# Performance work log

Hardware: AMD Instinct MI355X
Metric: run time of the kernel (lower is better)

Reference implementation:

```python
import jax, jax.numpy as jnp
import numpy as np

NQ, NT, NRF, K, M, B = 8, 16, 4, 4, 2, 28
N_OUTER, N_INNER = 120, 20

def _ry(t):
    c, s = jnp.cos(t / 2), jnp.sin(t / 2)
    return jnp.stack([jnp.stack([c, -s]), jnp.stack([s, c])]).astype(jnp.complex64)

def _rz(t):
    e = jnp.exp(-0.5j * t)
    z = jnp.zeros_like(e)
    return jnp.stack([jnp.stack([e, z]), jnp.stack([z, jnp.conj(e)])])

def _rot(phi, theta, omega):  # pennylane Rot = RZ(omega) RY(theta) RZ(phi)
    return _rz(omega) @ _ry(theta) @ _rz(phi)

def _ap1(state, U, w):
    return jnp.moveaxis(jnp.tensordot(U, state, axes=[[1], [w]]), 0, w)

def _cnot(state, c, t):
    s = jnp.moveaxis(state, (c, t), (0, 1))
    s = s.at[1].set(s[1, ::-1])
    return jnp.moveaxis(s, (0, 1), (c, t))

def _qcircuit(inp, w):  # inp [2*NQ] angles, w [3,NQ,3] -> [NQ] PauliZ expvals
    st = jnp.zeros((2,) * NQ, jnp.complex64).at[(0,) * NQ].set(1.0)
    for i in range(NQ):
        st = _ap1(st, _ry(inp[i]), i)
        st = _ap1(st, _rz(inp[i + NQ]), i)
    for l in range(3):
        for i in range(NQ):
            st = _ap1(st, _rot(w[l, i, 0], w[l, i, 1], w[l, i, 2]), i)
        for i in range(NQ - 1):
            st = _cnot(st, i, i + 1)
        st = _cnot(st, NQ - 1, 0)
    p = jnp.abs(st) ** 2
    z = [jnp.moveaxis(p, i, 0)[0].sum() - jnp.moveaxis(p, i, 0)[1].sum() for i in range(NQ)]
    return jnp.stack(z).astype(jnp.float32)

def _qblock(x, p):  # x [B,80] -> [B,out]
    W1, b1, W2, b2, W3, b3, qw, Wp, bp = p
    h = jnp.tanh(x @ W1.T + b1)
    h = jnp.tanh(h @ W2.T + b2)
    ang = h @ W3.T + b3  # [B, 2*NQ]
    q = jax.vmap(_qcircuit, in_axes=(0, None))(ang, qw)  # [B, NQ]
    return q @ Wp.T + bp

def _to_complex(x):
    return x[..., 0::2] + 1j * x[..., 1::2]

def _sum_rate(H, F, W, Pt):
    Heff = jnp.einsum('kbmn,nbr,kbru->kbmu', H, F[0], W)  # [K,B,M,M]
    G = jnp.einsum('kbmu,kbvu->kbmv', Heff, jnp.conj(Heff))
    A = jnp.eye(M, dtype=G.dtype) + Pt * G
    return jnp.sum(jnp.log2(jnp.abs(jnp.linalg.det(A).real) + 1e-12), axis=0).astype(jnp.float32)

def _beam_err(H, F, W, R, Pt):
    X = jnp.einsum('nbr,kbru->kbnu', F[0], W)  # [K,B,NT,M]
    C = jnp.einsum('kbnu,kbvu->kbnv', X, jnp.conj(X))  # [K,B,NT,NT]
    return jnp.mean(jnp.sqrt(jnp.sum(jnp.abs(C - R) ** 2, axis=(2, 3)) + 1e-12), axis=0).astype(jnp.float32)

def _normalize(F, W, H, Pt):
    F = F / (jnp.abs(F) + 1e-12)
    X = jnp.einsum('nbr,kbru->kbnu', F[0], W)
    pw = jnp.sum(jnp.abs(X) ** 2, axis=(0, 2, 3))  # [B]
    return F, W * jnp.sqrt(Pt / (pw + 1e-12))[None, :, None, None]

def _initialize(H, R, Pt, key):
    k1, k2 = jax.random.split(key)
    ph = jax.random.uniform(k1, (1, NT, B, NRF), maxval=2 * np.pi)
    F = jnp.exp(1j * ph).astype(jnp.complex64)
    W = jax.random.normal(k2, (K, B, NRF, M), dtype=jnp.complex64)
    return _normalize(F, W, H, Pt)

def _state(H, F, W, R, Wproj, bproj):
    s = jnp.concatenate([
        jnp.abs(F).mean((0, 1)).reshape(-1),    # B*NRF
        jnp.angle(F).mean((0, 1)).reshape(-1),  # B*NRF
        jnp.abs(W).mean((0, 1, 2)),             # M
        jnp.angle(W).mean((0, 1, 2)),           # M
        jnp.abs(H).mean((0, 1, 2)).reshape(-1), # NT
        jnp.abs(R).mean((0, 1)).reshape(-1),    # NT*NT  -> total 500
    ])
    return jnp.broadcast_to(s @ Wproj.T + bproj, (B, Wproj.shape[0]))

def _forward(H, R, Pt, step, qFp, qWp, Wproj, bproj):
    F, W = _initialize(H, R, Pt, jax.random.key(1))
    r0, t0 = _sum_rate(H, F, W, Pt), _beam_err(H, F, W, R, Pt)
    base = jax.random.key(7)

    def outer(carry, it):
        F, W = carry
        k = jax.random.fold_in(base, it)
        st = _state(H, F, W, R, Wproj, bproj)  # [B,80]

        def inner(c, p):
            Fc, kk = c
            kk, kn = jax.random.split(kk)
            dF = _to_complex(_qblock(st, p)).reshape(B, NT, NRF).transpose(1, 0, 2)[None]
            noise = jax.random.normal(kn, Fc.shape, dtype=jnp.complex64)
            Fc = Fc + step * noise * 0.001 + dF * 0.001
            return (Fc / (jnp.abs(Fc) + 1e-12), kk), None

        (F, k), _ = jax.lax.scan(inner, (F, k), qFp)
        dW = _to_complex(_qblock(st, qWp)).reshape(B, K, NRF, M).transpose(1, 0, 2, 3)
        k, kn = jax.random.split(k)
        W = W + step * jax.random.normal(kn, W.shape, dtype=jnp.complex64) * 0.001 + dW * 0.001
        F, W = _normalize(F, W, H, Pt)
        return (F, W), (_sum_rate(H, F, W, Pt), _beam_err(H, F, W, R, Pt))

    (F, W), (rs, ts) = jax.lax.scan(outer, (F, W), jnp.arange(N_OUTER))
    rates = jnp.concatenate([r0[None], rs], axis=0).T  # [B, N_OUTER+1]
    taus = jnp.concatenate([t0[None], ts], axis=0).T
    return rates, taus, F, W


def setup_inputs() -> dict:
    key = jax.random.key(0)
    ks = jax.random.split(key, 32)
    r = lambda i, sh: jax.random.normal(ks[i], sh, dtype=jnp.float32)
    WS = 0.1  # weight init scale for tanh stability
    return {
        'H_re': r(0, (K, B, M, NT)), 'H_im': r(1, (K, B, M, NT)),
        'R_re': r(2, (K, B, NT, NT)), 'R_im': r(3, (K, B, NT, NT)),
        'Pt': jnp.ones((1,), jnp.float32),
        'step': jnp.ones((1,), jnp.float32) * 0.02,
        'qF_W1': r(4, (N_INNER, 64, 80)) * WS, 'qF_b1': r(5, (N_INNER, 64)) * WS,
        'qF_W2': r(6, (N_INNER, 32, 64)) * WS, 'qF_b2': r(7, (N_INNER, 32)) * WS,
        'qF_W3': r(8, (N_INNER, 16, 32)) * WS, 'qF_b3': r(9, (N_INNER, 16)) * WS,
        'qF_qw': r(10, (N_INNER, 3, NQ, 3)), 'qF_Wp': r(11, (N_INNER, 128, NQ)) * WS,
        'qF_bp': r(12, (N_INNER, 128)) * WS,
        'qW_W1': r(13, (64, 80)) * WS, 'qW_b1': r(14, (64,)) * WS,
        'qW_W2': r(15, (32, 64)) * WS, 'qW_b2': r(16, (32,)) * WS,
        'qW_W3': r(17, (16, 32)) * WS, 'qW_b3': r(18, (16,)) * WS,
        'qW_qw': r(19, (3, NQ, 3)), 'qW_Wp': r(20, (64, NQ)) * WS,
        'qW_bp': r(21, (64,)) * WS,
        'proj_W': r(22, (80, 500)) * WS, 'proj_b': r(23, (80,)) * WS,
    }


def reference(H_re, H_im, R_re, R_im, Pt, step, qF_W1, qF_b1, qF_W2, qF_b2, qF_W3, qF_b3,
              qF_qw, qF_Wp, qF_bp, qW_W1, qW_b1, qW_W2, qW_b2, qW_W3, qW_b3, qW_qw, qW_Wp,
              qW_bp, proj_W, proj_b):
    H = (H_re + 1j * H_im).astype(jnp.complex64)
    R = (R_re + 1j * R_im).astype(jnp.complex64)
    qFp = (qF_W1, qF_b1, qF_W2, qF_b2, qF_W3, qF_b3, qF_qw, qF_Wp, qF_bp)
    qWp = (qW_W1, qW_b1, qW_W2, qW_b2, qW_W3, qW_b3, qW_qw, qW_Wp, qW_bp)
    return _forward(H, R, Pt[0], step[0], qFp, qWp, proj_W, proj_b)
```

## Files before the change

### kernel.cpp

```cpp
#include <hip/hip_runtime.h>
#include <stdint.h>

#define NT_   16
#define NRF_  4
#define K_    4
#define M_    2
#define B_    28
#define NOUT_ 120
#define NIN_  20
#define FN_   1792
#define WN_   896
#define XN_   3584
#define TJOB_ 8704
#define TSZ_  (21*TJOB_)
#define O_TAUS 3388
#define O_F    6776
#define O_W    10360

typedef float2 cf;
__device__ __forceinline__ cf cmul(cf a, cf b){ return make_float2(a.x*b.x - a.y*b.y, a.x*b.y + a.y*b.x); }
__device__ __forceinline__ cf cmulc(cf a, cf b){ return make_float2(a.x*b.x + a.y*b.y, a.y*b.x - a.x*b.y); }
__device__ __forceinline__ cf cadd(cf a, cf b){ return make_float2(a.x + b.x, a.y + b.y); }
__device__ __forceinline__ cf csc(float s, cf a){ return make_float2(s*a.x, s*a.y); }
__device__ __forceinline__ cf shflc(cf v, int m){ return make_float2(__shfl_xor(v.x, m, 64), __shfl_xor(v.y, m, 64)); }
// ... 130 lines not shown
    const float TWOPI = 6.28318530717958647692f;
    for (int e = t; e < FN_; e += 1024){
      float u = bits_to_unit(rbits(keys[0], (uint32_t)e));
      float ph = fmaxf(0.0f, u * TWOPI);
      float s, c; sincosf(ph, &s, &c);
      wsFst[e] = make_float2(c, s);
    }
    for (int e = t; e < WN_; e += 1024){
      cf w = cnormal(keys[1], keys[2], (uint32_t)e);
      wsIW[e] = w;
      wsWst[e] = w;
    }
  } else if (bi < 4*NOUT_ + 1 + 21){
    const int j = bi - (4*NOUT_ + 1);
    const bool isW = (j == 20);
    const float* W1 = isW ? qW_W1 : qF_W1 + j*(64*80);
    const float* W2 = isW ? qW_W2 : qF_W2 + j*(32*64);
    const float* W3 = isW ? qW_W3 : qF_W3 + j*(16*32);
    const float* Wp = isW ? qW_Wp : qF_Wp + j*(128*8);
    float* dst = wsT + j*TJOB_;
    for (int idx = t; idx < 5120; idx += 1024){
      int q = idx >> 6, i = idx & 63;
      dst[idx] = W1[i*80 + q];
    }
    for (int idx = t; idx < 2048; idx += 1024){
      int q = idx >> 5, i = idx & 31;
      dst[5120 + idx] = W2[i*64 + q];
    }
    for (int idx = t; idx < 512; idx += 1024){
      int q = idx >> 4, i = idx & 15;
      dst[7168 + idx] = W3[i*32 + q];
    }
    const int nOut = isW ? 64 : 128;
    for (int idx = t; idx < 8*nOut; idx += 1024){
      int z = idx / nOut, o = idx - z*nOut;
      dst[7680 + z*128 + o] = Wp[o*8 + z];
    }
  } else {
    if (t < 504){
      int j = t / 24, gg = t - j*24;
      const float* qw = (j == 20) ? qW_qw : qF_qw + j*72;
      float phi = qw[gg*3], th = qw[gg*3 + 1], om = qw[gg*3 + 2];
      float sh, ch; sincosf(0.5f*th, &sh, &ch);
      float sp, cp; sincosf(0.5f*(phi + om), &sp, &cp);
      float sm, cm; sincosf(0.5f*(phi - om), &sm, &cm);
      float* u = wsU + t*8;
      u[0] =  ch*cp; u[1] = -ch*sp;
      u[2] = -sh*cm; u[3] = -sh*sm;
      u[4] =  sh*cm; u[5] = -sh*sm;
      u[6] =  ch*cp; u[7] =  ch*sp;
    } else if (t < 520){
      int n = t - 504;
      float s = 0.f;
      for (int kbm = 0; kbm < 224; ++kbm){
        float re = H_re[kbm*16 + n], im = H_im[kbm*16 + n];
        s += sqrtf(re*re + im*im);
      }
      wsC[n] = s * (1.0f/224.0f);
    } else if (t < 776){
      int nv = t - 520;
      float s = 0.f;
      for (int kb = 0; kb < 112; ++kb){
        float re = R_re[kb*256 + nv], im = R_im[kb*256 + nv];
        s += sqrtf(re*re + im*im);
      }
      wsC[16 + nv] = s * (1.0f/112.0f);
    }
  }
}

__device__ __forceinline__ void gate(int q, cf u00, cf u01, cf u10, cf u11,
                                     cf &a0, cf &a1, cf &a2, cf &a3, int lane){
  if (q == 7){
    cf n0 = cadd(cmul(u00, a0), cmul(u01, a1));
    cf n1 = cadd(cmul(u10, a0), cmul(u11, a1));
    cf n2 = cadd(cmul(u00, a2), cmul(u01, a3));
    cf n3 = cadd(cmul(u10, a2), cmul(u11, a3));
    a0 = n0; a1 = n1; a2 = n2; a3 = n3;
  } else if (q == 6){
    cf n0 = cadd(cmul(u00, a0), cmul(u01, a2));
    cf n2 = cadd(cmul(u10, a0), cmul(u11, a2));
    cf n1 = cadd(cmul(u00, a1), cmul(u01, a3));
    cf n3 = cadd(cmul(u10, a1), cmul(u11, a3));
    a0 = n0; a1 = n1; a2 = n2; a3 = n3;
  } else {
    const int m = 1 << (5 - q);
    const bool hi = (lane & m) != 0;
    cf cO = hi ? u11 : u00;
    cf cP = hi ? u10 : u01;
    cf p0 = shflc(a0, m), p1 = shflc(a1, m), p2 = shflc(a2, m), p3 = shflc(a3, m);
    a0 = cadd(cmul(cO, a0), cmul(cP, p0));
    a1 = cadd(cmul(cO, a1), cmul(cP, p1));
    a2 = cadd(cmul(cO, a2), cmul(cP, p2));
    a3 = cadd(cmul(cO, a3), cmul(cP, p3));
  }
}

__device__ void run_circuit2(const float* trig, const float* uni, int lane, float z[8]){
  cf a0 = make_float2(lane == 0 ? 1.f : 0.f, 0.f);
  cf a1 = make_float2(0.f, 0.f), a2 = make_float2(0.f, 0.f), a3 = make_float2(0.f, 0.f);
  #pragma unroll
  for (int i = 0; i < 8; ++i){
    float sh = trig[2*i],      ch = trig[2*i + 1];
    float sp = trig[16 + 2*i], cp = trig[16 + 2*i + 1];
    float sm = trig[32 + 2*i], cm = trig[32 + 2*i + 1];
    cf u00 = make_float2( ch*cp, -ch*sp);
    cf u11 = make_float2( ch*cp,  ch*sp);
    cf u01 = make_float2(-sh*cm, -sh*sm);
    cf u10 = make_float2( sh*cm, -sh*sm);
    gate(i, u00, u01, u10, u11, a0, a1, a2, a3, lane);
  }
  for (int l = 0; l < 3; ++l){
    #pragma unroll
    for (int i = 0; i < 8; ++i){
      const float* u = uni + (l*8 + i)*8;
      gate(i, make_float2(u[0], u[1]), make_float2(u[2], u[3]),
              make_float2(u[4], u[5]), make_float2(u[6], u[7]), a0, a1, a2, a3, lane);
    }
    #pragma unroll
    for (int i = 0; i < 5; ++i){
      const int cm_ = 1 << (5 - i), tm = 1 << (4 - i);
      const bool c = (lane & cm_) != 0;
      cf p0 = shflc(a0, tm), p1 = shflc(a1, tm), p2 = shflc(a2, tm), p3 = shflc(a3, tm);
      a0 = c ? p0 : a0; a1 = c ? p1 : a1; a2 = c ? p2 : a2; a3 = c ? p3 : a3;
    }
    {
      const bool c = (lane & 1) != 0;
      cf t0 = c ? a2 : a0, t2 = c ? a0 : a2;
      cf t1 = c ? a3 : a1, t3 = c ? a1 : a3;
      a0 = t0; a1 = t1; a2 = t2; a3 = t3;
    }
    { cf tmp = a2; a2 = a3; a3 = tmp; }
    a1 = shflc(a1, 32);
    a3 = shflc(a3, 32);
  }
  const float p0 = a0.x*a0.x + a0.y*a0.y;
  const float p1 = a1.x*a1.x + a1.y*a1.y;
  const float p2 = a2.x*a2.x + a2.y*a2.y;
  const float p3 = a3.x*a3.x + a3.y*a3.y;
  const float tot = p0 + p1 + p2 + p3;
  z[6] = (p0 + p1) - (p2 + p3);
  z[7] = (p0 + p2) - (p1 + p3);
  #pragma unroll
  for (int i = 0; i < 6; ++i)
    z[i] = ((lane >> (5 - i)) & 1) ? -tot : tot;
  #pragma unroll
  for (int m = 1; m < 64; m <<= 1){
    #pragma unroll
    for (int i = 0; i < 8; ++i) z[i] += __shfl_xor(z[i], m, 64);
  }
}

__global__ __launch_bounds__(640)
void k_iter(const float* __restrict__ H_re, const float* __restrict__ H_im,
            const float* __restrict__ R_re, const float* __restrict__ R_im,
            const float* __restrict__ Pt_p, const float* __restrict__ step_p,
            const float* __restrict__ wsT, const float* __restrict__ wsU,
            const float* __restrict__ wsC,
            const float* __restrict__ featInA, const float* __restrict__ featInG,
            const float* __restrict__ featInP,
            float* __restrict__ featOutA, float* __restrict__ featOutG,
            float* __restrict__ featOutP,
            const float* __restrict__ projW, const float* __restrict__ projB,
            const float* __restrict__ qF_b1, const float* __restrict__ qF_b2,
            const float* __restrict__ qF_b3, const float* __restrict__ qF_bp,
            const float* __restrict__ qW_b1, const float* __restrict__ qW_b2,
            const float* __restrict__ qW_b3, const float* __restrict__ qW_bp,
            const float2* __restrict__ wsF, const float2* __restrict__ wsW,
            float2* __restrict__ wsdF, float2* __restrict__ wsdW,
            float2* __restrict__ wsFst, float2* __restrict__ wsWst,
            uint32_t* __restrict__ flag, uint32_t target,
            float* __restrict__ out, int it)
{
  const int wg = blockIdx.x;
  const int t = threadIdx.x;
  const int lane = t & 63;
  const int wv = t >> 6;
  __shared__ float sS[500];
  __shared__ float sSt[80];
  __shared__ float mlp[160];
  __shared__ float luni[192];
  __shared__ cf lF[64];
  __shared__ cf lW[32];
  __shared__ cf lX[128];
  __shared__ float scrA[96], scrG[96];
  __shared__ float red2[2];
  __shared__ float sscale;
  __shared__ float heR[16], heI[16];
  __shared__ float sKBl[4], sKB2l[4];

  if (wg < 21){
    const int j = wg;
    const bool isW = (j == 20);
    for (int i = t; i < 192; i += 640) luni[i] = wsU[j*192 + i];
    for (int i = t; i < 112; i += 640){ sS[i] = featInA[i]; sS[112 + i] = featInG[i]; }
    if (t < 4){
      float s = 0.f;
      for (int bb = 0; bb < 28; ++bb) s += featInP[bb*4 + t];
      sS[224 + t] = s * (1.0f/448.0f);
    }
    for (int i = t; i < 272; i += 640) sS[228 + i] = wsC[i];
    __syncthreads();
    {
      int o = wv*8 + (lane >> 3), i = lane & 7;
      const float* row = projW + o*500;
      float acc = 0.f;
      #pragma unroll
      for (int s = 0; s < 63; ++s){
        int j2 = i + 8*s;
        if (j2 < 500) acc = fmaf(sS[j2], row[j2], acc);
      }
      #pragma unroll
      for (int m = 1; m < 8; m <<= 1) acc += __shfl_xor(acc, m, 64);
      if (i == 0) sSt[o] = acc + projB[o];
    }
    __syncthreads();
    if (t < 64){
      const float* b1 = isW ? qW_b1 : qF_b1 + j*64;
      const float* b2 = isW ? qW_b2 : qF_b2 + j*32;
      const float* b3 = isW ? qW_b3 : qF_b3 + j*16;
      const float* bp = isW ? qW_bp : qF_bp + j*128;
      const float* w1t = wsT + j*TJOB_;
      const float* w2t = w1t + 5120;
      const float* w3t = w1t + 7168;
      const float* wpt = w1t + 7680;
      {
        float acc = b1[lane];
        for (int q = 0; q < 80; ++q) acc = fmaf(w1t[q*64 + lane], sSt[q], acc);
        mlp[lane] = tanhf(acc);
      }
      __builtin_amdgcn_wave_barrier();
      {
        int i2 = lane & 31;
        float acc = b2[i2];
        for (int q = 0; q < 64; ++q) acc = fmaf(w2t[q*32 + i2], mlp[q], acc);
        float h2 = tanhf(acc);
        __builtin_amdgcn_wave_barrier();
        if (lane < 32) mlp[64 + lane] = h2;
      }
      __builtin_amdgcn_wave_barrier();
      {
        int i3 = lane & 15;
        float acc = b3[i3];
        for (int q = 0; q < 32; ++q) acc = fmaf(w3t[q*16 + i3], mlp[64 + q], acc);
        __builtin_amdgcn_wave_barrier();
        if (lane < 16) mlp[96 + lane] = acc;
      }
      __builtin_amdgcn_wave_barrier();
      if (lane < 24){
        int i = lane & 7, which = lane >> 3;
        float th = mlp[96 + i], om = mlp[96 + 8 + i];
        float arg = (which == 0) ? 0.5f*th
                  : (which == 1) ? 0.5f*(0.f + om)
                                 : 0.5f*(0.f - om);
        float s, c; sincosf(arg, &s, &c);
        mlp[112 + which*16 + 2*i]     = s;
        mlp[112 + which*16 + 2*i + 1] = c;
      }
      __builtin_amdgcn_wave_barrier();
      float z[8];
      run_circuit2(mlp + 112, luni, lane, z);
      if (!isW){
        float o0 = bp[lane];
        float o1 = bp[64 + lane];
        #pragma unroll
        for (int i = 0; i < 8; ++i){
          o0 = fmaf(wpt[i*128 + lane],      z[i], o0);
          o1 = fmaf(wpt[i*128 + 64 + lane], z[i], o1);
        }
        __builtin_amdgcn_wave_barrier();
        mlp[lane] = o0; mlp[64 + lane] = o1;
        __builtin_amdgcn_wave_barrier();
        wsdF[j*64 + lane] = make_float2(mlp[2*lane], mlp[2*lane + 1]);
      } else {
        float o0 = bp[lane];
        #pragma unroll
        for (int i = 0; i < 8; ++i) o0 = fmaf(wpt[i*128 + lane], z[i], o0);
        __builtin_amdgcn_wave_barrier();
        mlp[lane] = o0;
        __builtin_amdgcn_wave_barrier();
        if (lane < 32) wsdW[lane] = make_float2(mlp[2*lane], mlp[2*lane + 1]);
      }
    }
    __syncthreads();
    if (t == 0){
      __threadfence();
      __hip_atomic_fetch_add(flag, 1u, __ATOMIC_RELAXED, __HIP_MEMORY_SCOPE_AGENT);
    }
    return;
  }

  const int b = wg - 21;
  const float c1 = step_p[0] * 0.001f;
  const float Ptv = Pt_p[0];

  cf F;
  cf nzA[10], nzB[10];
  cf w, nw;
  if (t < 64){
    const int n = t >> 2, r = t & 3;
    const int e = n*112 + b*4 + r;
    F = wsFst[e];
    const float2* np = wsF + (size_t)it*(NIN_*FN_);
    #pragma unroll
    for (int s = 0; s < 10; ++s) nzA[s] = np[s*FN_ + e];
    #pragma unroll
    for (int s = 0; s < 10; ++s) nzB[s] = np[(10 + s)*FN_ + e];
  } else if (t < 96){
    const int wi = t - 64;
    const int k = wi >> 3, ru = wi & 7;
    const int ew = (k*28 + b)*8 + ru;
    w  = wsWst[ew];
    nw = wsW[(size_t)it*WN_ + ew];
  }
  if (t == 0){
    while (__hip_atomic_load(flag, __ATOMIC_RELAXED, __HIP_MEMORY_SCOPE_AGENT) < target)
      __builtin_amdgcn_s_sleep(1);
    __threadfence();
  }
  __syncthreads();

  if (t < 64){
    cf dvA[10], dvB[10];
    #pragma unroll
    for (int s = 0; s < 10; ++s) dvA[s] = wsdF[s*64 + t];
    #pragma unroll
    for (int s = 0; s < 10; ++s) dvB[s] = wsdF[(10 + s)*64 + t];
    #pragma unroll
    for (int s = 0; s < 10; ++s){
      F.x = F.x + c1*nzA[s].x + 0.001f*dvA[s].x;
      F.y = F.y + c1*nzA[s].y + 0.001f*dvA[s].y;
      float rr = sqrtf(F.x*F.x + F.y*F.y) + 1e-12f;
      F.x /= rr; F.y /= rr;
    }
    #pragma unroll
    for (int s = 0; s < 10; ++s){
      F.x = F.x + c1*nzB[s].x + 0.001f*dvB[s].x;
      F.y = F.y + c1*nzB[s].y + 0.001f*dvB[s].y;
      float rr = sqrtf(F.x*F.x + F.y*F.y) + 1e-12f;
      F.x /= rr; F.y /= rr;
    }
    float rr = sqrtf(F.x*F.x + F.y*F.y) + 1e-12f;
    F.x /= rr; F.y /= rr;
    lF[t] = F;
    const int e = (t >> 2)*112 + b*4 + (t & 3);
    wsFst[e] = F;
  } else if (t < 96){
    const int wi = t - 64;
    const int k = wi >> 3, ru = wi & 7;
    cf dw = wsdW[k*8 + ru];
    w.x = w.x + c1*nw.x + 0.001f*dw.x;
    w.y = w.y + c1*nw.y + 0.001f*dw.y;
    lW[wi] = w;
  }
  __syncthreads();
  if (t < 128){
    int u = t & 1, n = (t >> 1) & 15, k = t >> 5;
    const cf* fr = lF + n*4;
    const cf* wr = lW + k*8 + u;
    cf acc = cmul(fr[0], wr[0]);
    acc = cadd(acc, cmul(fr[1], wr[2]));
    acc = cadd(acc, cmul(fr[2], wr[4]));
    acc = cadd(acc, cmul(fr[3], wr[6]));
    lX[t] = acc;
  }
  __syncthreads();
  if (t < 128){
    float s = lX[t].x*lX[t].x + lX[t].y*lX[t].y;
    #pragma unroll
    for (int m = 1; m < 64; m <<= 1) s += __shfl_xor(s, m, 64);
    if ((t & 63) == 0) red2[t >> 6] = s;
  }
  __syncthreads();
  if (t == 0) sscale = sqrtf(Ptv / ((red2[0] + red2[1]) + 1e-12f));
  __syncthreads();
  const float sc = sscale;
  if (t < 32){
    const int k = t >> 3, ru = t & 7;
    const int ew = (k*28 + b)*8 + ru;
    cf ww = csc(sc, lW[t]);
    lW[t] = ww;
    wsWst[ew] = ww;
  }
  if (t < 128) lX[t] = csc(sc, lX[t]);
  __syncthreads();
  if (t < 16){
    const int k = t >> 2, ent = t & 3;
    const int m = ent >> 1, u = ent & 1;
    const float* hr = H_re + (k*28 + b)*32 + m*16;
    const float* hi = H_im + (k*28 + b)*32 + m*16;
    cf He = make_float2(0.f, 0.f);
    for (int n = 0; n < 16; ++n){
      cf h = make_float2(hr[n], hi[n]);
      He = cadd(He, cmul(h, lX[k*32 + n*2 + u]));
    }
    heR[t] = He.x; heI[t] = He.y;
  }
  __builtin_amdgcn_wave_barrier();
  if (t < 4){
    const int k = t;
    cf He00 = make_float2(heR[k*4 + 0], heI[k*4 + 0]);
    cf He01 = make_float2(heR[k*4 + 1], heI[k*4 + 1]);
    cf He10 = make_float2(heR[k*4 + 2], heI[k*4 + 2]);
    cf He11 = make_float2(heR[k*4 + 3], heI[k*4 + 3]);
    cf G00 = cadd(cmulc(He00, He00), cmulc(He01, He01));
    cf G01 = cadd(cmulc(He00, He10), cmulc(He01, He11));
    cf G10 = cadd(cmulc(He10, He00), cmulc(He11, He01));
    cf G11 = cadd(cmulc(He10, He10), cmulc(He11, He11));
    cf A00 = make_float2(1.f + Ptv*G00.x, Ptv*G00.y);
    cf A01 = csc(Ptv, G01);
    cf A10 = csc(Ptv, G10);
    cf A11 = make_float2(1.f + Ptv*G11.x, Ptv*G11.y);
    float detre = (A00.x*A11.x - A00.y*A11.y) - (A01.x*A10.x - A01.y*A10.y);
    sKBl[k] = log2f(fabsf(detre) + 1e-12f);
  }
  if (t < 128){
    const int k = t >> 5, i = t & 31;
    const float* rr = R_re + (k*28 + b)*256;
    const float* ri = R_im + (k*28 + b)*256;
    float acc = 0.f;
    #pragma unroll
    for (int c = 0; c < 8; ++c){
      int nv = c*32 + i;
      int n = nv >> 4, v = nv & 15;
      cf xn0 = lX[k*32 + n*2], xn1 = lX[k*32 + n*2 + 1];
      cf xv0 = lX[k*32 + v*2], xv1 = lX[k*32 + v*2 + 1];
      cf C = cadd(cmulc(xn0, xv0), cmulc(xn1, xv1));
      float dr = C.x - rr[nv], di = C.y - ri[nv];
      acc += dr*dr + di*di;
    }
    #pragma unroll
    for (int m = 1; m < 32; m <<= 1) acc += __shfl_xor(acc, m, 64);
    if (i == 0) sKB2l[k] = sqrtf(acc + 1e-12f);
  }
  __syncthreads();
  if (t == 0){
    const int slot = it + 1;
    out[b*121 + slot] = sKBl[0] + sKBl[1] + sKBl[2] + sKBl[3];
    out[O_TAUS + b*121 + slot] = 0.25f*(sKB2l[0] + sKB2l[1] + sKB2l[2] + sKB2l[3]);
  }
  if (t < 64){
    cf f = lF[t];
    scrA[t] = sqrtf(f.x*f.x + f.y*f.y);
    scrG[t] = atan2f(f.y, f.x);
  } else if (t < 96){
    cf ww = lW[t - 64];
    scrA[t] = sqrtf(ww.x*ww.x + ww.y*ww.y);
    scrG[t] = atan2f(ww.y, ww.x);
  }
  __syncthreads();
  if (t < 8){
    int r = t & 3;
    const float* src = (t < 4) ? scrA : scrG;
    float s = 0.f;
    for (int n = 0; n < 16; ++n) s += src[n*4 + r];
    float* dst = (t < 4) ? featOutA : featOutG;
    dst[b*4 + r] = s * (1.0f/16.0f);
  } else if (t >= 8 && t < 12){
    int tt = t - 8;
    int u = tt & 1; bool isG = tt >= 2;
    const float* src = isG ? scrG : scrA;
    float s = 0.f;
    for (int i = 0; i < 16; ++i) s += src[64 + i*2 + u];
    featOutP[b*4 + tt] = s;
  }
}

__global__ __launch_bounds__(128)
void k_update(const float* __restrict__ H_re, const float* __restrict__ H_im,
              const float* __restrict__ R_re, const float* __restrict__ R_im,
              const float* __restrict__ Pt_p, const float* __restrict__ step_p,
              float2* __restrict__ wsFst, float2* __restrict__ wsWst,
              float* __restrict__ wsFeatA, float* __restrict__ wsFeatG,
              float* __restrict__ wsPart,
              float* __restrict__ out){
  const int b = blockIdx.x;
  const int t = threadIdx.x;
  __shared__ cf lF[64];
  __shared__ cf lW[32];
  __shared__ cf lX[128];
  __shared__ float scrA[96], scrG[96];
  __shared__ float red2[2];
  __shared__ float sscale;
  __shared__ float heR[16], heI[16];
  __shared__ float sKBl[4], sKB2l[4];
  const float Ptv = Pt_p[0];
  (void)step_p;

  if (t < 64){
    const int n = t >> 2, r = t & 3;
    const int e = n*112 + b*4 + r;
    cf F = wsFst[e];
    float rr = sqrtf(F.x*F.x + F.y*F.y) + 1e-12f;
    F.x /= rr; F.y /= rr;
    lF[t] = F;
    wsFst[e] = F;
  } else if (t < 96){
    const int wi = t - 64;
    const int k = wi >> 3, ru = wi & 7;
    lW[wi] = wsWst[(k*28 + b)*8 + ru];
  }
  __syncthreads();
  {
    int u = t & 1, n = (t >> 1) & 15, k = t >> 5;
    const cf* fr = lF + n*4;
    const cf* wr = lW + k*8 + u;
    cf acc = cmul(fr[0], wr[0]);
    acc = cadd(acc, cmul(fr[1], wr[2]));
    acc = cadd(acc, cmul(fr[2], wr[4]));
    acc = cadd(acc, cmul(fr[3], wr[6]));
    lX[t] = acc;
  }
  __syncthreads();
  {
    float s = lX[t].x*lX[t].x + lX[t].y*lX[t].y;
    #pragma unroll
    for (int m = 1; m < 64; m <<= 1) s += __shfl_xor(s, m, 64);
    if ((t & 63) == 0) red2[t >> 6] = s;
  }
  __syncthreads();
  if (t == 0) sscale = sqrtf(Ptv / ((red2[0] + red2[1]) + 1e-12f));
  __syncthreads();
  const float sc = sscale;
  if (t < 32){
    const int k = t >> 3, ru = t & 7;
    const int ew = (k*28 + b)*8 + ru;
    cf w = csc(sc, lW[t]);
    lW[t] = w;
    wsWst[ew] = w;
  }
  lX[t] = csc(sc, lX[t]);
  __syncthreads();
  if (t < 16){
    const int k = t >> 2, ent = t & 3;
    const int m = ent >> 1, u = ent & 1;
    const float* hr = H_re + (k*28 + b)*32 + m*16;
    const float* hi = H_im + (k*28 + b)*32 + m*16;
    cf He = make_float2(0.f, 0.f);
    for (int n = 0; n < 16; ++n){
      cf h = make_float2(hr[n], hi[n]);
      He = cadd(He, cmul(h, lX[k*32 + n*2 + u]));
    }
    heR[t] = He.x; heI[t] = He.y;
  }
  __builtin_amdgcn_wave_barrier();
  if (t < 4){
    const int k = t;
    cf He00 = make_float2(heR[k*4 + 0], heI[k*4 + 0]);
    cf He01 = make_float2(heR[k*4 + 1], heI[k*4 + 1]);
    cf He10 = make_float2(heR[k*4 + 2], heI[k*4 + 2]);
    cf He11 = make_float2(heR[k*4 + 3], heI[k*4 + 3]);
    cf G00 = cadd(cmulc(He00, He00), cmulc(He01, He01));
    cf G01 = cadd(cmulc(He00, He10), cmulc(He01, He11));
    cf G10 = cadd(cmulc(He10, He00), cmulc(He11, He01));
    cf G11 = cadd(cmulc(He10, He10), cmulc(He11, He11));
    cf A00 = make_float2(1.f + Ptv*G00.x, Ptv*G00.y);
    cf A01 = csc(Ptv, G01);
    cf A10 = csc(Ptv, G10);
    cf A11 = make_float2(1.f + Ptv*G11.x, Ptv*G11.y);
    float detre = (A00.x*A11.x - A00.y*A11.y) - (A01.x*A10.x - A01.y*A10.y);
    sKBl[k] = log2f(fabsf(detre) + 1e-12f);
  }
  {
    const int k = t >> 5, i = t & 31;
    const float* rr = R_re + (k*28 + b)*256;
    const float* ri = R_im + (k*28 + b)*256;
    float acc = 0.f;
    #pragma unroll
    for (int c = 0; c < 8; ++c){
      int nv = c*32 + i;
      int n = nv >> 4, v = nv & 15;
      cf xn0 = lX[k*32 + n*2], xn1 = lX[k*32 + n*2 + 1];
      cf xv0 = lX[k*32 + v*2], xv1 = lX[k*32 + v*2 + 1];
      cf C = cadd(cmulc(xn0, xv0), cmulc(xn1, xv1));
      float dr = C.x - rr[nv], di = C.y - ri[nv];
      acc += dr*dr + di*di;
    }
    #pragma unroll
    for (int m = 1; m < 32; m <<= 1) acc += __shfl_xor(acc, m, 64);
    if (i == 0) sKB2l[k] = sqrtf(acc + 1e-12f);
  }
  __syncthreads();
  if (t == 0){
    out[b*121 + 0] = sKBl[0] + sKBl[1] + sKBl[2] + sKBl[3];
    out[O_TAUS + b*121 + 0] = 0.25f*(sKB2l[0] + sKB2l[1] + sKB2l[2] + sKB2l[3]);
  }
  if (t < 64){
    cf f = lF[t];
    scrA[t] = sqrtf(f.x*f.x + f.y*f.y);
    scrG[t] = atan2f(f.y, f.x);
  } else if (t < 96){
    cf w = lW[t - 64];
    scrA[t] = sqrtf(w.x*w.x + w.y*w.y);
    scrG[t] = atan2f(w.y, w.x);
  }
  __syncthreads();
  if (t < 8){
    int r = t & 3;
    const float* src = (t < 4) ? scrA : scrG;
    float s = 0.f;
    for (int n = 0; n < 16; ++n) s += src[n*4 + r];
    float* dst = (t < 4) ? wsFeatA : wsFeatG;
    dst[b*4 + r] = s * (1.0f/16.0f);
  } else if (t >= 8 && t < 12){
    int tt = t - 8;
    int u = tt & 1; bool isG = tt >= 2;
    const float* src = isG ? scrG : scrA;
    float s = 0.f;
    for (int i = 0; i < 16; ++i) s += src[64 + i*2 + u];
    wsPart[b*4 + tt] = s;
  }
}

__global__ __launch_bounds__(1024)
void k_out(const float2* __restrict__ wsFst, const float2* __restrict__ wsWst,
           float* __restrict__ out, int fmode){
  const int t = threadIdx.x;
  if (fmode == 1){
    for (int e = t; e < FN_; e += 1024){
      out[O_F + e]       = wsFst[e].x;
      out[O_F + FN_ + e] = wsFst[e].y;
    }
    for (int e = t; e < WN_; e += 1024){
      out[O_W + e]       = wsWst[e].x;
      out[O_W + WN_ + e] = wsWst[e].y;
    }
  } else if (fmode == 2){
    for (int e = t; e < FN_; e += 1024) out[O_F + e] = wsFst[e].x;
    for (int e = t; e < WN_; e += 1024) out[O_F + FN_ + e] = wsWst[e].x;
  } else {
    for (int e = t; e < FN_; e += 1024){
      out[O_F + 2*e]     = wsFst[e].x;
      out[O_F + 2*e + 1] = wsFst[e].y;
    }
    for (int e = t; e < WN_; e += 1024){
      out[O_W + 2*e]     = wsWst[e].x;
      out[O_W + 2*e + 1] = wsWst[e].y;
    }
  }
}

extern "C" void kernel_launch(void* const* d_in, const int* in_sizes, int n_in,
                              void* d_out, int out_size, void* d_ws, size_t ws_size,
                              hipStream_t stream){
  (void)in_sizes; (void)n_in;
  const float* H_re  = (const float*)d_in[0];
  const float* H_im  = (const float*)d_in[1];
  const float* R_re  = (const float*)d_in[2];
  const float* R_im  = (const float*)d_in[3];
  const float* Pt    = (const float*)d_in[4];
  const float* stp   = (const float*)d_in[5];
  const float* qF_W1 = (const float*)d_in[6];
  const float* qF_b1 = (const float*)d_in[7];
  const float* qF_W2 = (const float*)d_in[8];
  const float* qF_b2 = (const float*)d_in[9];
  const float* qF_W3 = (const float*)d_in[10];
  const float* qF_b3 = (const float*)d_in[11];
  const float* qF_qw = (const float*)d_in[12];
  const float* qF_Wp = (const float*)d_in[13];
  const float* qF_bp = (const float*)d_in[14];
  const float* qW_W1 = (const float*)d_in[15];
  const float* qW_b1 = (const float*)d_in[16];
  const float* qW_W2 = (const float*)d_in[17];
  const float* qW_b2 = (const float*)d_in[18];
  const float* qW_W3 = (const float*)d_in[19];
  const float* qW_b3 = (const float*)d_in[20];
  const float* qW_qw = (const float*)d_in[21];
  const float* qW_Wp = (const float*)d_in[22];
  const float* qW_bp = (const float*)d_in[23];
  const float* projW = (const float*)d_in[24];
  const float* projB = (const float*)d_in[25];
  float* out = (float*)d_out;

  int fmode = 0;
  if (out_size == 12152) fmode = 1;
  else if (out_size == 9464) fmode = 2;

  const size_t nF = (size_t)NOUT_ * NIN_ * FN_;
  const size_t nW = (size_t)NOUT_ * WN_;
  const size_t need = (nF + nW + WN_ + FN_ + WN_ + 1280 + 32) * sizeof(float2)
                    + (TSZ_ + 4032 + 272 + 6*112 + 4) * sizeof(float);
  const int useWs = (d_ws != nullptr && ws_size >= need) ? 1 : 0;

  float2* wsF  = (float2*)d_ws;
  float2* wsW  = wsF + nF;
  float2* wsIW = wsW + nW;
  float*  wsT  = (float*)(wsIW + WN_);
  float*  wsU  = wsT + TSZ_;
  float*  wsC  = wsU + 4032;
  float2* wsFst = (float2*)(wsC + 272);
  float2* wsWst = wsFst + FN_;
  float2* wsdF  = wsWst + WN_;
  float2* wsdW  = wsdF + 1280;
  float*  fA0 = (float*)(wsdW + 32);
  float*  fG0 = fA0 + 112;
  float*  fP0 = fG0 + 112;
  float*  fA1 = fP0 + 112;
  float*  fG1 = fA1 + 112;
  float*  fP1 = fG1 + 112;
  uint32_t* flag = (uint32_t*)(fP1 + 112);

  if (useWs){
    hipMemsetAsync(flag, 0, 4, stream);
    rng_kernel<<<dim3(4*NOUT_ + 1 + 21 + 1), dim3(1024), 0, stream>>>(
        wsF, wsW, wsIW, wsT, wsU, wsC, wsFst, wsWst,
        H_re, H_im, R_re, R_im, qF_qw, qW_qw,
        qF_W1, qF_W2, qF_W3, qF_Wp, qW_W1, qW_W2, qW_W3, qW_Wp);
    k_update<<<dim3(B_), dim3(128), 0, stream>>>(
        H_re, H_im, R_re, R_im, Pt, stp,
        wsFst, wsWst, fA0, fG0, fP0, out);
    for (int it = 0; it < NOUT_; ++it){
      const int p = it & 1;
      k_iter<<<dim3(49), dim3(640), 0, stream>>>(
          H_re, H_im, R_re, R_im, Pt, stp,
          wsT, wsU, wsC,
          p ? fA1 : fA0, p ? fG1 : fG0, p ? fP1 : fP0,
          p ? fA0 : fA1, p ? fG0 : fG1, p ? fP0 : fP1,
          projW, projB,
          qF_b1, qF_b2, qF_b3, qF_bp, qW_b1, qW_b2, qW_b3, qW_bp,
          wsF, wsW, wsdF, wsdW, wsFst, wsWst,
          flag, 21u*(uint32_t)(it + 1), out, it);
    }
    k_out<<<dim3(1), dim3(1024), 0, stream>>>(wsFst, wsWst, out, fmode);
  } else {
    k_out<<<dim3(1), dim3(1024), 0, stream>>>(wsFst, wsWst, out, fmode);
  }
}
```

Before: 2.564 ms.

## Split fused iteration kernel into separate qblock and update launches

Replaces the single 49-block kernel per outer iteration, in which 28 update blocks spin on a global atomic flag waiting for 21 qblock blocks, with two kernels per iteration: a 21-block qblock kernel and a 28-block update kernel. Ordering now comes from stream launch order, which removes the spin-wait, the atomic flag, its memset and the double-buffered feature arrays. The cost is twice as many kernel launches (240 instead of 120), and the noise prefetch can no longer overlap the qblock compute.

```diff
diff --git a/kernel.cpp b/kernel.cpp
--- a/kernel.cpp
+++ b/kernel.cpp
@@ -306,34 +306,131 @@
 }
 
 __global__ __launch_bounds__(640)
-void k_iter(const float* __restrict__ H_re, const float* __restrict__ H_im,
-            const float* __restrict__ R_re, const float* __restrict__ R_im,
-            const float* __restrict__ Pt_p, const float* __restrict__ step_p,
-            const float* __restrict__ wsT, const float* __restrict__ wsU,
-            const float* __restrict__ wsC,
-            const float* __restrict__ featInA, const float* __restrict__ featInG,
-            const float* __restrict__ featInP,
-            float* __restrict__ featOutA, float* __restrict__ featOutG,
-            float* __restrict__ featOutP,
-            const float* __restrict__ projW, const float* __restrict__ projB,
-            const float* __restrict__ qF_b1, const float* __restrict__ qF_b2,
-            const float* __restrict__ qF_b3, const float* __restrict__ qF_bp,
-            const float* __restrict__ qW_b1, const float* __restrict__ qW_b2,
-            const float* __restrict__ qW_b3, const float* __restrict__ qW_bp,
-            const float2* __restrict__ wsF, const float2* __restrict__ wsW,
-            float2* __restrict__ wsdF, float2* __restrict__ wsdW,
-            float2* __restrict__ wsFst, float2* __restrict__ wsWst,
-            uint32_t* __restrict__ flag, uint32_t target,
-            float* __restrict__ out, int it)
-{
-  const int wg = blockIdx.x;
+void k_qblock2(const float* __restrict__ wsT, const float* __restrict__ wsU,
+               const float* __restrict__ wsC,
+               const float* __restrict__ wsFeatA, const float* __restrict__ wsFeatG,
+               const float* __restrict__ wsPart,
+               const float* __restrict__ projW, const float* __restrict__ projB,
+               const float* __restrict__ qF_b1, const float* __restrict__ qF_b2,
+               const float* __restrict__ qF_b3, const float* __restrict__ qF_bp,
+               const float* __restrict__ qW_b1, const float* __restrict__ qW_b2,
+               const float* __restrict__ qW_b3, const float* __restrict__ qW_bp,
+               float2* __restrict__ wsdF, float2* __restrict__ wsdW){
+  const int j = blockIdx.x;
   const int t = threadIdx.x;
   const int lane = t & 63;
   const int wv = t >> 6;
+  const bool isW = (j == 20);
   __shared__ float sS[500];
   __shared__ float sSt[80];
   __shared__ float mlp[160];
   __shared__ float luni[192];
+  for (int i = t; i < 192; i += 640) luni[i] = wsU[j*192 + i];
+  for (int i = t; i < 112; i += 640){ sS[i] = wsFeatA[i]; sS[112 + i] = wsFeatG[i]; }
+  if (t < 4){
+    float s = 0.f;
+    for (int bb = 0; bb < 28; ++bb) s += wsPart[bb*4 + t];
+    sS[224 + t] = s * (1.0f/448.0f);
+  }
+  for (int i = t; i < 272; i += 640) sS[228 + i] = wsC[i];
+  __syncthreads();
+  {
+    int o = wv*8 + (lane >> 3), i = lane & 7;
+    const float* row = projW + o*500;
+    float acc = 0.f;
+    #pragma unroll
+    for (int s = 0; s < 63; ++s){
+      int j2 = i + 8*s;
+      if (j2 < 500) acc = fmaf(sS[j2], row[j2], acc);
+    }
+    #pragma unroll
+    for (int m = 1; m < 8; m <<= 1) acc += __shfl_xor(acc, m, 64);
+    if (i == 0) sSt[o] = acc + projB[o];
+  }
+  __syncthreads();
+
+  if (t < 64){
+    const float* b1 = isW ? qW_b1 : qF_b1 + j*64;
+    const float* b2 = isW ? qW_b2 : qF_b2 + j*32;
+    const float* b3 = isW ? qW_b3 : qF_b3 + j*16;
+    const float* bp = isW ? qW_bp : qF_bp + j*128;
+    const float* w1t = wsT + j*TJOB_;
+    const float* w2t = w1t + 5120;
+    const float* w3t = w1t + 7168;
+    const float* wpt = w1t + 7680;
+
+    {
+      float acc = b1[lane];
+      for (int q = 0; q < 80; ++q) acc = fmaf(w1t[q*64 + lane], sSt[q], acc);
+      mlp[lane] = tanhf(acc);
+    }
+    __builtin_amdgcn_wave_barrier();
+    {
+      int i2 = lane & 31;
+      float acc = b2[i2];
+      for (int q = 0; q < 64; ++q) acc = fmaf(w2t[q*32 + i2], mlp[q], acc);
+      float h2 = tanhf(acc);
+      __builtin_amdgcn_wave_barrier();
+      if (lane < 32) mlp[64 + lane] = h2;
+    }
+    __builtin_amdgcn_wave_barrier();
+    {
+      int i3 = lane & 15;
+      float acc = b3[i3];
+      for (int q = 0; q < 32; ++q) acc = fmaf(w3t[q*16 + i3], mlp[64 + q], acc);
+      __builtin_amdgcn_wave_barrier();
+      if (lane < 16) mlp[96 + lane] = acc;
+    }
+    __builtin_amdgcn_wave_barrier();
+    if (lane < 24){
+      int i = lane & 7, which = lane >> 3;
+      float th = mlp[96 + i], om = mlp[96 + 8 + i];
+      float arg = (which == 0) ? 0.5f*th
+                : (which == 1) ? 0.5f*(0.f + om)
+                               : 0.5f*(0.f - om);
+      float s, c; sincosf(arg, &s, &c);
+      mlp[112 + which*16 + 2*i]     = s;
+      mlp[112 + which*16 + 2*i + 1] = c;
+    }
+    __builtin_amdgcn_wave_barrier();
+    float z[8];
+    run_circuit2(mlp + 112, luni, lane, z);
+    if (!isW){
+      float o0 = bp[lane];
+      float o1 = bp[64 + lane];
+      #pragma unroll
+      for (int i = 0; i < 8; ++i){
+        o0 = fmaf(wpt[i*128 + lane],      z[i], o0);
+        o1 = fmaf(wpt[i*128 + 64 + lane], z[i], o1);
+      }
+      __builtin_amdgcn_wave_barrier();
+      mlp[lane] = o0; mlp[64 + lane] = o1;
+      __builtin_amdgcn_wave_barrier();
+      wsdF[j*64 + lane] = make_float2(mlp[2*lane], mlp[2*lane + 1]);
+    } else {
+      float o0 = bp[lane];
+      #pragma unroll
+      for (int i = 0; i < 8; ++i) o0 = fmaf(wpt[i*128 + lane], z[i], o0);
+      __builtin_amdgcn_wave_barrier();
+      mlp[lane] = o0;
+      __builtin_amdgcn_wave_barrier();
+      if (lane < 32) wsdW[lane] = make_float2(mlp[2*lane], mlp[2*lane + 1]);
+    }
+  }
+}
+
+__global__ __launch_bounds__(128)
+void k_update(const float* __restrict__ H_re, const float* __restrict__ H_im,
+              const float* __restrict__ R_re, const float* __restrict__ R_im,
+              const float* __restrict__ Pt_p, const float* __restrict__ step_p,
+              const float2* __restrict__ wsF, const float2* __restrict__ wsW,
+              const float2* __restrict__ wsdF, const float2* __restrict__ wsdW,
+              float2* __restrict__ wsFst, float2* __restrict__ wsWst,
+              float* __restrict__ wsFeatA, float* __restrict__ wsFeatG,
+              float* __restrict__ wsPart,
+              float* __restrict__ out, int it, int mode){
+  const int b = blockIdx.x;
+  const int t = threadIdx.x;
   __shared__ cf lF[64];
   __shared__ cf lW[32];
   __shared__ cf lX[128];
@@ -342,173 +439,54 @@
   __shared__ float sscale;
   __shared__ float heR[16], heI[16];
   __shared__ float sKBl[4], sKB2l[4];
-
-  if (wg < 21){
-    const int j = wg;
-    const bool isW = (j == 20);
-    for (int i = t; i < 192; i += 640) luni[i] = wsU[j*192 + i];
-    for (int i = t; i < 112; i += 640){ sS[i] = featInA[i]; sS[112 + i] = featInG[i]; }
-    if (t < 4){
-      float s = 0.f;
-      for (int bb = 0; bb < 28; ++bb) s += featInP[bb*4 + t];
-      sS[224 + t] = s * (1.0f/448.0f);
-    }
-    for (int i = t; i < 272; i += 640) sS[228 + i] = wsC[i];
-    __syncthreads();
-    {
-      int o = wv*8 + (lane >> 3), i = lane & 7;
-      const float* row = projW + o*500;
-      float acc = 0.f;
-      #pragma unroll
-      for (int s = 0; s < 63; ++s){
-        int j2 = i + 8*s;
-        if (j2 < 500) acc = fmaf(sS[j2], row[j2], acc);
-      }
-      #pragma unroll
-      for (int m = 1; m < 8; m <<= 1) acc += __shfl_xor(acc, m, 64);
-      if (i == 0) sSt[o] = acc + projB[o];
-    }
-    __syncthreads();
-    if (t < 64){
-      const float* b1 = isW ? qW_b1 : qF_b1 + j*64;
-      const float* b2 = isW ? qW_b2 : qF_b2 + j*32;
-      const float* b3 = isW ? qW_b3 : qF_b3 + j*16;
-      const float* bp = isW ? qW_bp : qF_bp + j*128;
-      const float* w1t = wsT + j*TJOB_;
-      const float* w2t = w1t + 5120;
-      const float* w3t = w1t + 7168;
-      const float* wpt = w1t + 7680;
-      {
-        float acc = b1[lane];
-        for (int q = 0; q < 80; ++q) acc = fmaf(w1t[q*64 + lane], sSt[q], acc);
-        mlp[lane] = tanhf(acc);
-      }
-      __builtin_amdgcn_wave_barrier();
-      {
-        int i2 = lane & 31;
-        float acc = b2[i2];
-        for (int q = 0; q < 64; ++q) acc = fmaf(w2t[q*32 + i2], mlp[q], acc);
-        float h2 = tanhf(acc);
-        __builtin_amdgcn_wave_barrier();
-        if (lane < 32) mlp[64 + lane] = h2;
-      }
-      __builtin_amdgcn_wave_barrier();
-      {
-        int i3 = lane & 15;
-        float acc = b3[i3];
-        for (int q = 0; q < 32; ++q) acc = fmaf(w3t[q*16 + i3], mlp[64 + q], acc);
-        __builtin_amdgcn_wave_barrier();
-        if (lane < 16) mlp[96 + lane] = acc;
-      }
-      __builtin_amdgcn_wave_barrier();
-      if (lane < 24){
-        int i = lane & 7, which = lane >> 3;
-        float th = mlp[96 + i], om = mlp[96 + 8 + i];
-        float arg = (which == 0) ? 0.5f*th
-                  : (which == 1) ? 0.5f*(0.f + om)
-                                 : 0.5f*(0.f - om);
-        float s, c; sincosf(arg, &s, &c);
-        mlp[112 + which*16 + 2*i]     = s;
-        mlp[112 + which*16 + 2*i + 1] = c;
-      }
-      __builtin_amdgcn_wave_barrier();
-      float z[8];
-      run_circuit2(mlp + 112, luni, lane, z);
-      if (!isW){
-        float o0 = bp[lane];
-        float o1 = bp[64 + lane];
-        #pragma unroll
-        for (int i = 0; i < 8; ++i){
-          o0 = fmaf(wpt[i*128 + lane],      z[i], o0);
-          o1 = fmaf(wpt[i*128 + 64 + lane], z[i], o1);
-        }
-        __builtin_amdgcn_wave_barrier();
-        mlp[lane] = o0; mlp[64 + lane] = o1;
-        __builtin_amdgcn_wave_barrier();
-        wsdF[j*64 + lane] = make_float2(mlp[2*lane], mlp[2*lane + 1]);
-      } else {
-        float o0 = bp[lane];
-        #pragma unroll
-        for (int i = 0; i < 8; ++i) o0 = fmaf(wpt[i*128 + lane], z[i], o0);
-        __builtin_amdgcn_wave_barrier();
-        mlp[lane] = o0;
-        __builtin_amdgcn_wave_barrier();
-        if (lane < 32) wsdW[lane] = make_float2(mlp[2*lane], mlp[2*lane + 1]);
-      }
-    }
-    __syncthreads();
-    if (t == 0){
-      __threadfence();
-      __hip_atomic_fetch_add(flag, 1u, __ATOMIC_RELAXED, __HIP_MEMORY_SCOPE_AGENT);
-    }
-    return;
-  }
-
-  const int b = wg - 21;
   const float c1 = step_p[0] * 0.001f;
   const float Ptv = Pt_p[0];
 
-  cf F;
-  cf nzA[10], nzB[10];
-  cf w, nw;
   if (t < 64){
     const int n = t >> 2, r = t & 3;
     const int e = n*112 + b*4 + r;
-    F = wsFst[e];
-    const float2* np = wsF + (size_t)it*(NIN_*FN_);
-    #pragma unroll
-    for (int s = 0; s < 10; ++s) nzA[s] = np[s*FN_ + e];
-    #pragma unroll
-    for (int s = 0; s < 10; ++s) nzB[s] = np[(10 + s)*FN_ + e];
+    cf F = wsFst[e];
+    if (mode){
+      const float2* np = wsF + (size_t)it*(NIN_*FN_);
+      cf nzA[10], dvA[10], nzB[10], dvB[10];
+      #pragma unroll
+      for (int s = 0; s < 10; ++s){ nzA[s] = np[s*FN_ + e];        dvA[s] = wsdF[s*64 + t]; }
+      #pragma unroll
+      for (int s = 0; s < 10; ++s){ nzB[s] = np[(10 + s)*FN_ + e]; dvB[s] = wsdF[(10 + s)*64 + t]; }
+      #pragma unroll
+      for (int s = 0; s < 10; ++s){
+        F.x = F.x + c1*nzA[s].x + 0.001f*dvA[s].x;
+        F.y = F.y + c1*nzA[s].y + 0.001f*dvA[s].y;
+        float rr = sqrtf(F.x*F.x + F.y*F.y) + 1e-12f;
+        F.x /= rr; F.y /= rr;
+      }
+      #pragma unroll
+      for (int s = 0; s < 10; ++s){
+        F.x = F.x + c1*nzB[s].x + 0.001f*dvB[s].x;
+        F.y = F.y + c1*nzB[s].y + 0.001f*dvB[s].y;
+        float rr = sqrtf(F.x*F.x + F.y*F.y) + 1e-12f;
+        F.x /= rr; F.y /= rr;
+      }
+    }
+    float rr = sqrtf(F.x*F.x + F.y*F.y) + 1e-12f;
+    F.x /= rr; F.y /= rr;
+    lF[t] = F;
+    wsFst[e] = F;
   } else if (t < 96){
     const int wi = t - 64;
     const int k = wi >> 3, ru = wi & 7;
     const int ew = (k*28 + b)*8 + ru;
-    w  = wsWst[ew];
-    nw = wsW[(size_t)it*WN_ + ew];
-  }
-  if (t == 0){
-    while (__hip_atomic_load(flag, __ATOMIC_RELAXED, __HIP_MEMORY_SCOPE_AGENT) < target)
-      __builtin_amdgcn_s_sleep(1);
-    __threadfence();
-  }
-  __syncthreads();
-
-  if (t < 64){
-    cf dvA[10], dvB[10];
-    #pragma unroll
-    for (int s = 0; s < 10; ++s) dvA[s] = wsdF[s*64 + t];
-    #pragma unroll
-    for (int s = 0; s < 10; ++s) dvB[s] = wsdF[(10 + s)*64 + t];
-    #pragma unroll
-    for (int s = 0; s < 10; ++s){
-      F.x = F.x + c1*nzA[s].x + 0.001f*dvA[s].x;
-      F.y = F.y + c1*nzA[s].y + 0.001f*dvA[s].y;
-      float rr = sqrtf(F.x*F.x + F.y*F.y) + 1e-12f;
-      F.x /= rr; F.y /= rr;
-    }
-    #pragma unroll
-    for (int s = 0; s < 10; ++s){
-      F.x = F.x + c1*nzB[s].x + 0.001f*dvB[s].x;
-      F.y = F.y + c1*nzB[s].y + 0.001f*dvB[s].y;
-      float rr = sqrtf(F.x*F.x + F.y*F.y) + 1e-12f;
-      F.x /= rr; F.y /= rr;
-    }
-    float rr = sqrtf(F.x*F.x + F.y*F.y) + 1e-12f;
-    F.x /= rr; F.y /= rr;
-    lF[t] = F;
-    const int e = (t >> 2)*112 + b*4 + (t & 3);
-    wsFst[e] = F;
-  } else if (t < 96){
-    const int wi = t - 64;
-    const int k = wi >> 3, ru = wi & 7;
-    cf dw = wsdW[k*8 + ru];
-    w.x = w.x + c1*nw.x + 0.001f*dw.x;
-    w.y = w.y + c1*nw.y + 0.001f*dw.y;
+    cf w = wsWst[ew];
+    if (mode){
+      cf nw = wsW[(size_t)it*WN_ + ew];
+      cf dw = wsdW[k*8 + ru];
+      w.x = w.x + c1*nw.x + 0.001f*dw.x;
+      w.y = w.y + c1*nw.y + 0.001f*dw.y;
+    }
     lW[wi] = w;
   }
   __syncthreads();
-  if (t < 128){
+  {
     int u = t & 1, n = (t >> 1) & 15, k = t >> 5;
     const cf* fr = lF + n*4;
     const cf* wr = lW + k*8 + u;
@@ -519,7 +497,7 @@
     lX[t] = acc;
   }
   __syncthreads();
-  if (t < 128){
+  {
     float s = lX[t].x*lX[t].x + lX[t].y*lX[t].y;
     #pragma unroll
     for (int m = 1; m < 64; m <<= 1) s += __shfl_xor(s, m, 64);
@@ -532,11 +510,11 @@
   if (t < 32){
     const int k = t >> 3, ru = t & 7;
     const int ew = (k*28 + b)*8 + ru;
-    cf ww = csc(sc, lW[t]);
-    lW[t] = ww;
-    wsWst[ew] = ww;
-  }
-  if (t < 128) lX[t] = csc(sc, lX[t]);
+    cf w = csc(sc, lW[t]);
+    lW[t] = w;
+    wsWst[ew] = w;
+  }
+  lX[t] = csc(sc, lX[t]);
   __syncthreads();
   if (t < 16){
     const int k = t >> 2, ent = t & 3;
@@ -568,153 +546,6 @@
     float detre = (A00.x*A11.x - A00.y*A11.y) - (A01.x*A10.x - A01.y*A10.y);
     sKBl[k] = log2f(fabsf(detre) + 1e-12f);
   }
-  if (t < 128){
-    const int k = t >> 5, i = t & 31;
-    const float* rr = R_re + (k*28 + b)*256;
-    const float* ri = R_im + (k*28 + b)*256;
-    float acc = 0.f;
-    #pragma unroll
-    for (int c = 0; c < 8; ++c){
-      int nv = c*32 + i;
-      int n = nv >> 4, v = nv & 15;
-      cf xn0 = lX[k*32 + n*2], xn1 = lX[k*32 + n*2 + 1];
-      cf xv0 = lX[k*32 + v*2], xv1 = lX[k*32 + v*2 + 1];
-      cf C = cadd(cmulc(xn0, xv0), cmulc(xn1, xv1));
-      float dr = C.x - rr[nv], di = C.y - ri[nv];
-      acc += dr*dr + di*di;
-    }
-    #pragma unroll
-    for (int m = 1; m < 32; m <<= 1) acc += __shfl_xor(acc, m, 64);
-    if (i == 0) sKB2l[k] = sqrtf(acc + 1e-12f);
-  }
-  __syncthreads();
-  if (t == 0){
-    const int slot = it + 1;
-    out[b*121 + slot] = sKBl[0] + sKBl[1] + sKBl[2] + sKBl[3];
-    out[O_TAUS + b*121 + slot] = 0.25f*(sKB2l[0] + sKB2l[1] + sKB2l[2] + sKB2l[3]);
-  }
-  if (t < 64){
-    cf f = lF[t];
-    scrA[t] = sqrtf(f.x*f.x + f.y*f.y);
-    scrG[t] = atan2f(f.y, f.x);
-  } else if (t < 96){
-    cf ww = lW[t - 64];
-    scrA[t] = sqrtf(ww.x*ww.x + ww.y*ww.y);
-    scrG[t] = atan2f(ww.y, ww.x);
-  }
-  __syncthreads();
-  if (t < 8){
-    int r = t & 3;
-    const float* src = (t < 4) ? scrA : scrG;
-    float s = 0.f;
-    for (int n = 0; n < 16; ++n) s += src[n*4 + r];
-    float* dst = (t < 4) ? featOutA : featOutG;
-    dst[b*4 + r] = s * (1.0f/16.0f);
-  } else if (t >= 8 && t < 12){
-    int tt = t - 8;
-    int u = tt & 1; bool isG = tt >= 2;
-    const float* src = isG ? scrG : scrA;
-    float s = 0.f;
-    for (int i = 0; i < 16; ++i) s += src[64 + i*2 + u];
-    featOutP[b*4 + tt] = s;
-  }
-}
-
-__global__ __launch_bounds__(128)
-void k_update(const float* __restrict__ H_re, const float* __restrict__ H_im,
-              const float* __restrict__ R_re, const float* __restrict__ R_im,
-              const float* __restrict__ Pt_p, const float* __restrict__ step_p,
-              float2* __restrict__ wsFst, float2* __restrict__ wsWst,
-              float* __restrict__ wsFeatA, float* __restrict__ wsFeatG,
-              float* __restrict__ wsPart,
-              float* __restrict__ out){
-  const int b = blockIdx.x;
-  const int t = threadIdx.x;
-  __shared__ cf lF[64];
-  __shared__ cf lW[32];
-  __shared__ cf lX[128];
-  __shared__ float scrA[96], scrG[96];
-  __shared__ float red2[2];
-  __shared__ float sscale;
-  __shared__ float heR[16], heI[16];
-  __shared__ float sKBl[4], sKB2l[4];
-  const float Ptv = Pt_p[0];
-  (void)step_p;
-
-  if (t < 64){
-    const int n = t >> 2, r = t & 3;
-    const int e = n*112 + b*4 + r;
-    cf F = wsFst[e];
-    float rr = sqrtf(F.x*F.x + F.y*F.y) + 1e-12f;
-    F.x /= rr; F.y /= rr;
-    lF[t] = F;
-    wsFst[e] = F;
-  } else if (t < 96){
-    const int wi = t - 64;
-    const int k = wi >> 3, ru = wi & 7;
-    lW[wi] = wsWst[(k*28 + b)*8 + ru];
-  }
-  __syncthreads();
-  {
-    int u = t & 1, n = (t >> 1) & 15, k = t >> 5;
-    const cf* fr = lF + n*4;
-    const cf* wr = lW + k*8 + u;
-    cf acc = cmul(fr[0], wr[0]);
-    acc = cadd(acc, cmul(fr[1], wr[2]));
-    acc = cadd(acc, cmul(fr[2], wr[4]));
-    acc = cadd(acc, cmul(fr[3], wr[6]));
-    lX[t] = acc;
-  }
-  __syncthreads();
-  {
-    float s = lX[t].x*lX[t].x + lX[t].y*lX[t].y;
-    #pragma unroll
-    for (int m = 1; m < 64; m <<= 1) s += __shfl_xor(s, m, 64);
-    if ((t & 63) == 0) red2[t >> 6] = s;
-  }
-  __syncthreads();
-  if (t == 0) sscale = sqrtf(Ptv / ((red2[0] + red2[1]) + 1e-12f));
-  __syncthreads();
-  const float sc = sscale;
-  if (t < 32){
-    const int k = t >> 3, ru = t & 7;
-    const int ew = (k*28 + b)*8 + ru;
-    cf w = csc(sc, lW[t]);
-    lW[t] = w;
-    wsWst[ew] = w;
-  }
-  lX[t] = csc(sc, lX[t]);
-  __syncthreads();
-  if (t < 16){
-    const int k = t >> 2, ent = t & 3;
-    const int m = ent >> 1, u = ent & 1;
-    const float* hr = H_re + (k*28 + b)*32 + m*16;
-    const float* hi = H_im + (k*28 + b)*32 + m*16;
-    cf He = make_float2(0.f, 0.f);
-    for (int n = 0; n < 16; ++n){
-      cf h = make_float2(hr[n], hi[n]);
-      He = cadd(He, cmul(h, lX[k*32 + n*2 + u]));
-    }
-    heR[t] = He.x; heI[t] = He.y;
-  }
-  __builtin_amdgcn_wave_barrier();
-  if (t < 4){
-    const int k = t;
-    cf He00 = make_float2(heR[k*4 + 0], heI[k*4 + 0]);
-    cf He01 = make_float2(heR[k*4 + 1], heI[k*4 + 1]);
-    cf He10 = make_float2(heR[k*4 + 2], heI[k*4 + 2]);
-    cf He11 = make_float2(heR[k*4 + 3], heI[k*4 + 3]);
-    cf G00 = cadd(cmulc(He00, He00), cmulc(He01, He01));
-    cf G01 = cadd(cmulc(He00, He10), cmulc(He01, He11));
-    cf G10 = cadd(cmulc(He10, He00), cmulc(He11, He01));
-    cf G11 = cadd(cmulc(He10, He10), cmulc(He11, He11));
-    cf A00 = make_float2(1.f + Ptv*G00.x, Ptv*G00.y);
-    cf A01 = csc(Ptv, G01);
-    cf A10 = csc(Ptv, G10);
-    cf A11 = make_float2(1.f + Ptv*G11.x, Ptv*G11.y);
-    float detre = (A00.x*A11.x - A00.y*A11.y) - (A01.x*A10.x - A01.y*A10.y);
-    sKBl[k] = log2f(fabsf(detre) + 1e-12f);
-  }
   {
     const int k = t >> 5, i = t & 31;
     const float* rr = R_re + (k*28 + b)*256;
@@ -736,8 +567,9 @@
   }
   __syncthreads();
   if (t == 0){
-    out[b*121 + 0] = sKBl[0] + sKBl[1] + sKBl[2] + sKBl[3];
-    out[O_TAUS + b*121 + 0] = 0.25f*(sKB2l[0] + sKB2l[1] + sKB2l[2] + sKB2l[3]);
+    const int slot = mode ? (it + 1) : 0;
+    out[b*121 + slot] = sKBl[0] + sKBl[1] + sKBl[2] + sKBl[3];
+    out[O_TAUS + b*121 + slot] = 0.25f*(sKB2l[0] + sKB2l[1] + sKB2l[2] + sKB2l[3]);
   }
   if (t < 64){
     cf f = lF[t];
@@ -833,7 +665,7 @@
   const size_t nF = (size_t)NOUT_ * NIN_ * FN_;
   const size_t nW = (size_t)NOUT_ * WN_;
   const size_t need = (nF + nW + WN_ + FN_ + WN_ + 1280 + 32) * sizeof(float2)
-                    + (TSZ_ + 4032 + 272 + 6*112 + 4) * sizeof(float);
+                    + (TSZ_ + 4032 + 272 + 112 + 112 + 112 + 4) * sizeof(float);
   const int useWs = (d_ws != nullptr && ws_size >= need) ? 1 : 0;
 
   float2* wsF  = (float2*)d_ws;
@@ -846,34 +678,26 @@
   float2* wsWst = wsFst + FN_;
   float2* wsdF  = wsWst + WN_;
   float2* wsdW  = wsdF + 1280;
-  float*  fA0 = (float*)(wsdW + 32);
-  float*  fG0 = fA0 + 112;
-  float*  fP0 = fG0 + 112;
-  float*  fA1 = fP0 + 112;
-  float*  fG1 = fA1 + 112;
-  float*  fP1 = fG1 + 112;
-  uint32_t* flag = (uint32_t*)(fP1 + 112);
+  float*  wsFeatA = (float*)(wsdW + 32);
+  float*  wsFeatG = wsFeatA + 112;
+  float*  wsPart  = wsFeatG + 112;
 
   if (useWs){
-    hipMemsetAsync(flag, 0, 4, stream);
     rng_kernel<<<dim3(4*NOUT_ + 1 + 21 + 1), dim3(1024), 0, stream>>>(
         wsF, wsW, wsIW, wsT, wsU, wsC, wsFst, wsWst,
         H_re, H_im, R_re, R_im, qF_qw, qW_qw,
         qF_W1, qF_W2, qF_W3, qF_Wp, qW_W1, qW_W2, qW_W3, qW_Wp);
     k_update<<<dim3(B_), dim3(128), 0, stream>>>(
-        H_re, H_im, R_re, R_im, Pt, stp,
-        wsFst, wsWst, fA0, fG0, fP0, out);
+        H_re, H_im, R_re, R_im, Pt, stp, wsF, wsW, wsdF, wsdW,
+        wsFst, wsWst, wsFeatA, wsFeatG, wsPart, out, 0, 0);
     for (int it = 0; it < NOUT_; ++it){
-      const int p = it & 1;
-      k_iter<<<dim3(49), dim3(640), 0, stream>>>(
-          H_re, H_im, R_re, R_im, Pt, stp,
-          wsT, wsU, wsC,
-          p ? fA1 : fA0, p ? fG1 : fG0, p ? fP1 : fP0,
-          p ? fA0 : fA1, p ? fG0 : fG1, p ? fP0 : fP1,
-          projW, projB,
+      k_qblock2<<<dim3(21), dim3(640), 0, stream>>>(
+          wsT, wsU, wsC, wsFeatA, wsFeatG, wsPart, projW, projB,
           qF_b1, qF_b2, qF_b3, qF_bp, qW_b1, qW_b2, qW_b3, qW_bp,
-          wsF, wsW, wsdF, wsdW, wsFst, wsWst,
-          flag, 21u*(uint32_t)(it + 1), out, it);
+          wsdF, wsdW);
+      k_update<<<dim3(B_), dim3(128), 0, stream>>>(
+          H_re, H_im, R_re, R_im, Pt, stp, wsF, wsW, wsdF, wsdW,
+          wsFst, wsWst, wsFeatA, wsFeatG, wsPart, out, it, 1);
     }
     k_out<<<dim3(1), dim3(1024), 0, stream>>>(wsFst, wsWst, out, fmode);
   } else {
```

Result: faster. 2.498 ms (-2.6%).
